# Kernel optimization log

Hardware: AMD Instinct MI355X
Metric: run time of the kernel (lower is better)

## Reference

```python
import jax, jax.numpy as jnp
import numpy as np
import math

INPUT_SIZE = 1024
B, L1, L2 = 8, 2048, 2048


def setup_inputs() -> dict:
    key = jax.random.key(0)
    ks = jax.random.split(key, 10)
    s = 1.0 / math.sqrt(INPUT_SIZE)
    return {
        "Q": jax.random.normal(ks[0], (B, L1, INPUT_SIZE), dtype=jnp.float32),
        "K": jax.random.normal(ks[1], (B, L2, INPUT_SIZE), dtype=jnp.float32),
        "V": jax.random.normal(ks[2], (B, L2, INPUT_SIZE), dtype=jnp.float32),
        "K_mask": jax.random.randint(ks[3], (B, L2), 0, 2, dtype=jnp.int32),
        "Wq": jax.random.normal(ks[4], (INPUT_SIZE, INPUT_SIZE), dtype=jnp.float32) * s,
        "bq": jax.random.normal(ks[5], (INPUT_SIZE,), dtype=jnp.float32) * s,
        "Wk": jax.random.normal(ks[6], (INPUT_SIZE, INPUT_SIZE), dtype=jnp.float32) * s,
        "bk": jax.random.normal(ks[7], (INPUT_SIZE,), dtype=jnp.float32) * s,
        "Wv": jax.random.normal(ks[8], (INPUT_SIZE, INPUT_SIZE), dtype=jnp.float32) * s,
        "bv": jax.random.normal(ks[9], (INPUT_SIZE,), dtype=jnp.float32) * s,
    }


def reference(Q, K, V, K_mask, Wq, bq, Wk, bk, Wv, bv):
    # Linear projections (torch Linear: x @ W.T + b)
    q = jnp.einsum('bld,ed->ble', Q, Wq) + bq
    k = jnp.einsum('bld,ed->ble', K, Wk) + bk
    v = jnp.einsum('bld,ed->ble', V, Wv) + bv
    # scores: [B, L1, L2], scaled by sqrt(input_size)
    scores = jnp.einsum('bqd,bkd->bqk', q, k) / math.sqrt(INPUT_SIZE)
    # K_mask == 1 marks padding -> -inf before softmax
    scores = jnp.where(K_mask[:, None, :] == 1, -jnp.inf, scores)
    alpha = jax.nn.softmax(scores, axis=-1)
    matched_seq = jnp.einsum('bqk,bkd->bqd', alpha, v)
    return matched_seq
```

## Files before the change

### kernel.cpp

```cpp
#include <hip/hip_runtime.h>


using u16 = unsigned short;
using frag_ab = __attribute__((ext_vector_type(8))) short;
using frag_cd = __attribute__((ext_vector_type(4))) float;

#define BAR() asm volatile("s_barrier" ::: "memory")
#define WAITV(n) asm volatile("s_waitcnt vmcnt(" #n ")" ::: "memory")
#define WAITLGKM0() do { asm volatile("s_waitcnt lgkmcnt(0)" ::: "memory"); \
                         __builtin_amdgcn_sched_barrier(0); } while (0)
#define HINT_LGKM8() asm volatile("s_waitcnt lgkmcnt(8)" ::: "memory")
#define L(d, ab, h) (lds + (((d) * 4) + ((ab) * 2) + (h)) * 8192)

__device__ __forceinline__ u16 f2bf(float f) {
  union { float f; unsigned u; } c; c.f = f;
  unsigned u = c.u;
  return (u16)((u + 0x7FFFu + ((u >> 16) & 1u)) >> 16);
}
__device__ __forceinline__ u16 f2h(float f) {
  union { _Float16 h; u16 u; } c; c.h = (_Float16)f; return c.u;
}
__device__ __forceinline__ float h2f(u16 u) {
  union { u16 u; _Float16 h; } c; c.u = u; return (float)c.h;
}

__device__ __forceinline__ void async_ld16(const void* g, void* l) {
  __builtin_amdgcn_global_load_lds(
      (const __attribute__((address_space(1))) unsigned*)g,
      (__attribute__((address_space(3))) unsigned*)l, 16, 0, 0);
}

__global__ void cvtw3(const float* __restrict__ a, const float* __restrict__ b,
                      const float* __restrict__ c, u16* __restrict__ out) {
  const float* in = blockIdx.z == 0 ? a : (blockIdx.z == 1 ? b : c);
  u16* o = out + (long)blockIdx.z * 1048576L;
  long i = ((long)blockIdx.x * 256 + threadIdx.x) * 4;
  float4 v = *reinterpret_cast<const float4*>(in + i);
  *reinterpret_cast<ushort4*>(o + i) =
      make_ushort4(f2bf(v.x), f2bf(v.y), f2bf(v.z), f2bf(v.w));
}

__global__ void cvt3_f32_bf16(const float* __restrict__ q, const float* __restrict__ k,
                              const float* __restrict__ v, u16* __restrict__ out) {
  const float* in = blockIdx.z == 0 ? q : (blockIdx.z == 1 ? k : v);
  u16* o = out + (long)blockIdx.z * 16777216L;
  long i = ((long)blockIdx.x * 256 + threadIdx.x) * 4;
  float4 x = *reinterpret_cast<const float4*>(in + i);
  *reinterpret_cast<ushort4*>(o + i) =
      make_ushort4(f2bf(x.x), f2bf(x.y), f2bf(x.z), f2bf(x.w));
}

__device__ __forceinline__ void stage_half(const u16* __restrict__ g_rowbase,
                                           long Kstr, u16* l_half,
                                           int wave, int lane) {
  const int t = wave * 64 + lane;
  #pragma unroll
  for (int i = 0; i < 2; i++) {
    const int row = i * 64 + (t >> 3);
    const int cb  = (t & 7) * 16;
    const int cbs = cb ^ ((row & 7) << 4);
    async_ld16(g_rowbase + (long)row * Kstr + (cbs >> 1),
               l_half + i * 4096 + wave * 512);
  }
}

__device__ __forceinline__ frag_ab ld_frag(const u16* half_base, int r, int k) {
  const int idx = r * 64 + (k ^ ((r & 7) << 3));
  return *reinterpret_cast<const frag_ab*>(half_base + idx);
}

struct SwzOut { int z, m0, n0; };
__device__ __forceinline__ SwzOut grid_swizzle() {
  const int gx = gridDim.x, gy = gridDim.y, gz = gridDim.z;
  const int nwg = gx * gy * gz;
  const int lin = ((int)blockIdx.z * gy + blockIdx.y) * gx + blockIdx.x;
  const int q8 = nwg >> 3, r8 = nwg & 7;
  const int xcd = lin & 7, idx8 = lin >> 3;
  const int swz = (xcd < r8 ? xcd * (q8 + 1) : r8 * (q8 + 1) + (xcd - r8) * q8) + idx8;
  SwzOut o;
  o.z = swz / (gx * gy);
  const int rem = swz % (gx * gy);
  o.m0 = (rem / gx) * 256;
  o.n0 = (rem % gx) * 256;
  return o;
}

__device__ __forceinline__ void
gemm256_core(int out_mode, const u16* __restrict__ Ab, const u16* __restrict__ Bb,
             void* __restrict__ Cb, const float* __restrict__ bias,
             int N, int K, int m0, int n0, float scale, u16* lds)
{
  const int tid = threadIdx.x;
  const int wave = tid >> 6, lane = tid & 63;
  const int wm = wave >> 2, wn = wave & 3;
  const int ln15 = lane & 15, kof = (lane >> 4) * 8;
  const int rB0 = (wn & 1) * 64;
  const int NT = K >> 6;

  frag_cd acc[8][4];
  #pragma unroll
  for (int i = 0; i < 8; i++)
    #pragma unroll
    for (int j = 0; j < 4; j++)
      acc[i][j] = (frag_cd){0.f, 0.f, 0.f, 0.f};

  stage_half(Ab + (long)(m0 +   0) * K, K, L(0, 0, 0), wave, lane);
  stage_half(Ab + (long)(m0 + 128) * K, K, L(0, 0, 1), wave, lane);
  stage_half(Bb + (long)(n0 +   0) * K, K, L(0, 1, 0), wave, lane);
  stage_half(Bb + (long)(n0 + 128) * K, K, L(0, 1, 1), wave, lane);
  {
    const int t1 = (1 < NT) ? 1 : 0;
    stage_half(Bb + (long)(n0 +   0) * K + t1 * 64, K, L(1, 1, 0), wave, lane);
    stage_half(Bb + (long)(n0 + 128) * K + t1 * 64, K, L(1, 1, 1), wave, lane);
  }
  WAITV(4);
  BAR();

  for (int t = 0; t < NT; ++t) {
    const int d = t & 1;
    const u16* Al = L(d, 0, wm);
    const u16* Bl = L(d, 1, wn >> 1);
    const int tA = (t + 1 < NT) ? t + 1 : NT - 1;
    const int tB = (t + 2 < NT) ? t + 2 : NT - 1;

    frag_ab bf[4][2], af[2][2];

    #pragma unroll
    for (int bn = 0; bn < 4; ++bn)
      #pragma unroll
      for (int kk = 0; kk < 2; ++kk)
        bf[bn][kk] = ld_frag(Bl, rB0 + bn * 16 + ln15, kk * 32 + kof);
    #pragma unroll
    for (int am = 0; am < 2; ++am)
      #pragma unroll
      for (int kk = 0; kk < 2; ++kk)
        af[am][kk] = ld_frag(Al, am * 16 + ln15, kk * 32 + kof);
    stage_half(Ab + (long)(m0 + 0) * K + tA * 64, K, L(d ^ 1, 0, 0), wave, lane);
    HINT_LGKM8();
    BAR();
    __builtin_amdgcn_s_setprio(1);
    #pragma unroll
    for (int am = 0; am < 2; ++am)
      #pragma unroll
      for (int bn = 0; bn < 4; ++bn)
        #pragma unroll
        for (int kk = 0; kk < 2; ++kk)
          acc[am][bn] = __builtin_amdgcn_mfma_f32_16x16x32_bf16(af[am][kk], bf[bn][kk], acc[am][bn], 0, 0, 0);
    __builtin_amdgcn_s_setprio(0);
    BAR();

    #pragma unroll
    for (int am = 0; am < 2; ++am)
      #pragma unroll
      for (int kk = 0; kk < 2; ++kk)
        af[am][kk] = ld_frag(Al, (2 + am) * 16 + ln15, kk * 32 + kof);
    stage_half(Ab + (long)(m0 + 128) * K + tA * 64, K, L(d ^ 1, 0, 1), wave, lane);
    BAR();
    __builtin_amdgcn_s_setprio(1);
    #pragma unroll
    for (int am = 0; am < 2; ++am)
      #pragma unroll
      for (int bn = 0; bn < 4; ++bn)
        #pragma unroll
        for (int kk = 0; kk < 2; ++kk)
          acc[2 + am][bn] = __builtin_amdgcn_mfma_f32_16x16x32_bf16(af[am][kk], bf[bn][kk], acc[2 + am][bn], 0, 0, 0);
    __builtin_amdgcn_s_setprio(0);
    BAR();

    #pragma unroll
    for (int am = 0; am < 2; ++am)
      #pragma unroll
      for (int kk = 0; kk < 2; ++kk)
        af[am][kk] = ld_frag(Al, (4 + am) * 16 + ln15, kk * 32 + kof);
    stage_half(Bb + (long)(n0 + 0) * K + tB * 64, K, L(d, 1, 0), wave, lane);
    BAR();
    __builtin_amdgcn_s_setprio(1);
    #pragma unroll
    for (int am = 0; am < 2; ++am)
      #pragma unroll
      for (int bn = 0; bn < 4; ++bn)
        #pragma unroll
        for (int kk = 0; kk < 2; ++kk)
          acc[4 + am][bn] = __builtin_amdgcn_mfma_f32_16x16x32_bf16(af[am][kk], bf[bn][kk], acc[4 + am][bn], 0, 0, 0);
    __builtin_amdgcn_s_setprio(0);
    BAR();

    #pragma unroll
    for (int am = 0; am < 2; ++am)
      #pragma unroll
      for (int kk = 0; kk < 2; ++kk)
        af[am][kk] = ld_frag(Al, (6 + am) * 16 + ln15, kk * 32 + kof);
    stage_half(Bb + (long)(n0 + 128) * K + tB * 64, K, L(d, 1, 1), wave, lane);
    BAR();
    __builtin_amdgcn_s_setprio(1);
    #pragma unroll
    for (int am = 0; am < 2; ++am)
      #pragma unroll
      for (int bn = 0; bn < 4; ++bn)
        #pragma unroll
        for (int kk = 0; kk < 2; ++kk)
          acc[6 + am][bn] = __builtin_amdgcn_mfma_f32_16x16x32_bf16(af[am][kk], bf[bn][kk], acc[6 + am][bn], 0, 0, 0);
    __builtin_amdgcn_s_setprio(0);
    WAITV(4);
    BAR();
  }

  WAITV(0);
  BAR();

  const int cl = lane & 15;
  const int rb = (lane >> 4) * 4;

  if (out_mode == 1 || out_mode == 3) {
    u16* Wt = lds + wave * 8192;
    #pragma unroll
    for (int am = 0; am < 8; ++am)
      #pragma unroll
      for (int bn = 0; bn < 4; ++bn) {
        const int col = bn * 16 + cl;
        const float badd = bias ? bias[n0 + wn * 64 + col] : 0.f;
        #pragma unroll
        for (int r = 0; r < 4; ++r) {
          const int row = am * 16 + rb + r;
          const int slot = (col >> 3) ^ ((row >> 2) & 7);
          const float val = acc[am][bn][r] * scale + badd;
          Wt[row * 64 + slot * 8 + (col & 7)] = (out_mode == 1) ? f2bf(val) : f2h(val);
        }
      }
    WAITLGKM0();
    u16* Cp = (u16*)Cb;
    #pragma unroll
    for (int i = 0; i < 16; ++i) {
      const int row = (lane >> 3) + i * 8;
      const int c = lane & 7;
      const int slot = c ^ ((row >> 2) & 7);
      frag_ab v = *reinterpret_cast<const frag_ab*>(Wt + row * 64 + slot * 8);
      const long grow = m0 + wm * 128 + row;
      const int gcol = n0 + wn * 64 + c * 8;
      *reinterpret_cast<frag_ab*>(Cp + grow * N + gcol) = v;
    }
  } else if (out_mode == 0) {
    float* Wt = (float*)(void*)lds + wave * 4096;
    float* Cp = (float*)Cb;
    #pragma unroll
    for (int p = 0; p < 2; ++p) {
      #pragma unroll
      for (int am = 0; am < 8; ++am)
        #pragma unroll
        for (int bn = 0; bn < 2; ++bn) {
          const int col = bn * 16 + cl;
          #pragma unroll
          for (int r = 0; r < 4; ++r) {
            const int row = am * 16 + rb + r;
            const int slot = (col >> 2) ^ ((row >> 2) & 7);
            Wt[row * 32 + slot * 4 + (col & 3)] = acc[am][2 * p + bn][r] * scale;
          }
        }
      WAITLGKM0();
      #pragma unroll
      for (int i = 0; i < 16; ++i) {
        const int row = (lane >> 3) + i * 8;
        const int c = lane & 7;
        const int slot = c ^ ((row >> 2) & 7);
        float4 v = *reinterpret_cast<const float4*>(Wt + row * 32 + slot * 4);
        const long grow = m0 + wm * 128 + row;
        const int gcol = n0 + wn * 64 + p * 32 + c * 4;
        *reinterpret_cast<float4*>(Cp + grow * N + gcol) = v;
      }
      if (p == 0) WAITLGKM0();
    }
  } else {
    #pragma unroll
    for (int bn = 0; bn < 4; ++bn) {
      const int gcol = n0 + wn * 64 + bn * 16 + cl;
      const float badd = bias ? bias[gcol] : 0.f;
      #pragma unroll
      for (int am = 0; am < 8; ++am) {
        const int grow0 = m0 + wm * 128 + am * 16 + rb;
        ushort4 pk;
        pk.x = f2bf(acc[am][bn][0] * scale + badd);
        pk.y = f2bf(acc[am][bn][1] * scale + badd);
        pk.z = f2bf(acc[am][bn][2] * scale + badd);
        pk.w = f2bf(acc[am][bn][3] * scale + badd);
        const int bb = grow0 >> 11, l2 = grow0 & 2047;
        *reinterpret_cast<ushort4*>((u16*)Cb + ((long)bb * N + gcol) * 2048L + l2) = pk;
      }
    }
  }
}

__global__ void __launch_bounds__(512, 2)
proj3_gemm(const u16* __restrict__ X, const u16* __restrict__ Wb,
           const float* __restrict__ bq, const float* __restrict__ bk,
           const float* __restrict__ bv, u16* __restrict__ qkb,
           u16* __restrict__ vT)
{
  __shared__ u16 lds[8 * 8192];
  SwzOut s = grid_swizzle();
  const u16* A = X + (long)s.z * 16777216L;
  const u16* W = Wb + (long)s.z * 1048576L;
  const float* bias = s.z == 0 ? bq : (s.z == 1 ? bk : bv);
  if (s.z < 2)
    gemm256_core(1, A, W, qkb + (long)s.z * 16777216L, bias,
                 1024, 1024, s.m0, s.n0, 1.f, lds);
  else
    gemm256_core(2, A, W, vT, bias, 1024, 1024, s.m0, s.n0, 1.f, lds);
}

__global__ void __launch_bounds__(512, 2)
proj1_gemm(int mode, const u16* A, const u16* W, void* C, const float* bias) {
  __shared__ u16 lds[8 * 8192];
  SwzOut s = grid_swizzle();
  gemm256_core(mode, A, W, C, bias, 1024, 1024, s.m0, s.n0, 1.f, lds);
}

__global__ void __launch_bounds__(512, 2)
qk_gemm(const u16* A, const u16* Bt, void* C,
        int M, int N, int K, long sA, long sB, long sC, float scale) {
  __shared__ u16 lds[8 * 8192];
  SwzOut s = grid_swizzle();
  gemm256_core(3, A + (long)s.z * sA, Bt + (long)s.z * sB,
               (u16*)C + (long)s.z * sC, nullptr, N, K, s.m0, s.n0, scale, lds);
}
__global__ void __launch_bounds__(512, 2)
pv_gemm(const u16* A, const u16* Bt, void* C,
        int M, int N, int K, long sA, long sB, long sC, float scale) {
  __shared__ u16 lds[8 * 8192];
  SwzOut s = grid_swizzle();
  gemm256_core(0, A + (long)s.z * sA, Bt + (long)s.z * sB,
               (float*)C + (long)s.z * sC, nullptr, N, K, s.m0, s.n0, scale, lds);
}

__global__ void softmax_rows_h(const u16* __restrict__ S, const int* __restrict__ Km,
                               u16* __restrict__ P)
{
  const long row = blockIdx.x;
  const int b = (int)(row >> 11);
  const u16* s = S + row * 2048;
  const int* mask = Km + (long)b * 2048;
  u16* p = P + row * 2048;

  const int t = threadIdx.x;
  const int base = t * 8;

  ushort4 r0 = *reinterpret_cast<const ushort4*>(s + base);
  ushort4 r1 = *reinterpret_cast<const ushort4*>(s + base + 4);
  int4 mA = *reinterpret_cast<const int4*>(mask + base);
  int4 mB = *reinterpret_cast<const int4*>(mask + base + 4);

  float vals[8] = {h2f(r0.x), h2f(r0.y), h2f(r0.z), h2f(r0.w),
                   h2f(r1.x), h2f(r1.y), h2f(r1.z), h2f(r1.w)};
  const int mk[8] = {mA.x, mA.y, mA.z, mA.w, mB.x, mB.y, mB.z, mB.w};

  float mx = -3.0e38f;
  #pragma unroll
  for (int i = 0; i < 8; i++) if (!mk[i]) mx = fmaxf(mx, vals[i]);
  #pragma unroll
  for (int off = 32; off > 0; off >>= 1) mx = fmaxf(mx, __shfl_xor(mx, off));

  __shared__ float redm[4], reds[4];
  const int wave = t >> 6, lane = t & 63;
  if (lane == 0) redm[wave] = mx;
  __syncthreads();
  mx = fmaxf(fmaxf(redm[0], redm[1]), fmaxf(redm[2], redm[3]));

  float e[8]; float sum = 0.f;
  #pragma unroll
  for (int i = 0; i < 8; i++) { e[i] = mk[i] ? 0.f : __expf(vals[i] - mx); sum += e[i]; }
  #pragma unroll
  for (int off = 32; off > 0; off >>= 1) sum += __shfl_xor(sum, off);
  if (lane == 0) reds[wave] = sum;
  __syncthreads();
  sum = reds[0] + reds[1] + reds[2] + reds[3];
  const float inv = 1.f / sum;

  *reinterpret_cast<ushort4*>(p + base) =
      make_ushort4(f2bf(e[0]*inv), f2bf(e[1]*inv), f2bf(e[2]*inv), f2bf(e[3]*inv));
  *reinterpret_cast<ushort4*>(p + base + 4) =
      make_ushort4(f2bf(e[4]*inv), f2bf(e[5]*inv), f2bf(e[6]*inv), f2bf(e[7]*inv));
}

extern "C" void kernel_launch(void* const* d_in, const int* in_sizes, int n_in,
                              void* d_out, int out_size, void* d_ws, size_t ws_size,
                              hipStream_t stream) {
  (void)in_sizes; (void)n_in; (void)out_size;

  const float* Qin  = (const float*)d_in[0];
  const float* Kin  = (const float*)d_in[1];
  const float* Vin  = (const float*)d_in[2];
  const int*   Kmask = (const int*)d_in[3];
  const float* Wq = (const float*)d_in[4];
  const float* bq = (const float*)d_in[5];
  const float* Wk = (const float*)d_in[6];
  const float* bk = (const float*)d_in[7];
  const float* Wv = (const float*)d_in[8];
  const float* bv = (const float*)d_in[9];

  char* ws = (char*)d_ws;
  const size_t MB = 1024UL * 1024UL;
  const dim3 blk(256);
  const dim3 gblk(512);
  const float rs = 0.03125f;

  if (ws_size >= 226 * MB) {
    u16*  qb = (u16*)(ws);
    u16*  vT = (u16*)(ws + 64 * MB);
    u16*  P  = (u16*)(ws + 96 * MB);
    u16*  Xq = (u16*)(ws + 96 * MB);
    u16*  S  = (u16*)(ws + 160 * MB);
    u16*  Wb = (u16*)(ws + 224 * MB);

    cvt3_f32_bf16<<<dim3(16384, 1, 3), blk, 0, stream>>>(Qin, Kin, Vin, Xq);
    cvtw3<<<dim3(1024, 1, 3), blk, 0, stream>>>(Wq, Wk, Wv, Wb);

    proj3_gemm<<<dim3(4, 64, 3), gblk, 0, stream>>>(Xq, Wb, bq, bk, bv, qb, vT);

    qk_gemm<<<dim3(8, 8, 8), gblk, 0, stream>>>(qb, qb + 16777216L, S,
        2048, 2048, 1024, 2048L * 1024, 2048L * 1024, 2048L * 2048, rs);
    softmax_rows_h<<<dim3(16384), blk, 0, stream>>>(S, Kmask, P);

    pv_gemm<<<dim3(4, 8, 8), gblk, 0, stream>>>(P, vT, d_out,
        2048, 1024, 2048, 2048L * 2048, 1024L * 2048, 2048L * 1024, 1.f);
  } else if (ws_size >= 194 * MB) {
    u16*  qb = (u16*)(ws);
    u16*  vT = (u16*)(ws + 64 * MB);
    u16*  P  = (u16*)(ws + 96 * MB);
    u16*  Xq = (u16*)(ws + 96 * MB);
    u16*  S  = (u16*)(ws + 160 * MB);
    u16*  Wb = (u16*)(ws + 186 * MB);

    cvt3_f32_bf16<<<dim3(16384, 1, 3), blk, 0, stream>>>(Qin, Kin, Vin, Xq);
    cvtw3<<<dim3(1024, 1, 3), blk, 0, stream>>>(Wq, Wk, Wv, Wb);

    proj3_gemm<<<dim3(4, 64, 3), gblk, 0, stream>>>(Xq, Wb, bq, bk, bv, qb, vT);

    for (int h = 0; h < 2; h++) {
      const u16* qbH = qb + (long)(4 * h) * 2048 * 1024;
      const u16* kbH = qb + 16777216L + (long)(4 * h) * 2048 * 1024;
      qk_gemm<<<dim3(8, 8, 4), gblk, 0, stream>>>(qbH, kbH, S,
          2048, 2048, 1024, 2048L * 1024, 2048L * 1024, 2048L * 2048, rs);
      softmax_rows_h<<<dim3(8192), blk, 0, stream>>>(
          S, Kmask + (long)(4 * h) * 2048, P + (long)(4 * h) * 2048 * 2048);
    }

    pv_gemm<<<dim3(4, 8, 8), gblk, 0, stream>>>(P, vT, d_out,
        2048, 1024, 2048, 2048L * 2048, 1024L * 2048, 2048L * 1024, 1.f);
  } else {
    u16*  qb = (u16*)(ws);
    u16*  kb = (u16*)(ws + 32 * MB);
    u16*  vT = (u16*)(ws + 64 * MB);
    u16*  Xb = (u16*)(ws + 96 * MB);
    u16*  S  = (u16*)(ws + 96 * MB);
    u16*  P  = (u16*)(ws + 104 * MB);
    u16*  Wb = (u16*)(ws + 128 * MB);

    cvtw3<<<dim3(1024, 1, 3), blk, 0, stream>>>(Wq, Wk, Wv, Wb);
    cvt3_f32_bf16<<<dim3(16384, 1, 1), blk, 0, stream>>>(Qin, Qin, Qin, Xb);
    proj1_gemm<<<dim3(4, 64, 1), gblk, 0, stream>>>(1, Xb, Wb, qb, bq);
    cvt3_f32_bf16<<<dim3(16384, 1, 1), blk, 0, stream>>>(Kin, Kin, Kin, Xb);
    proj1_gemm<<<dim3(4, 64, 1), gblk, 0, stream>>>(1, Xb, Wb + 1048576L, kb, bk);
    cvt3_f32_bf16<<<dim3(16384, 1, 1), blk, 0, stream>>>(Vin, Vin, Vin, Xb);
    proj1_gemm<<<dim3(4, 64, 1), gblk, 0, stream>>>(2, Xb, Wb + 2L * 1048576L, vT, bv);

    for (int b = 0; b < 8; b++) {
      const u16* qbB = qb + (long)b * 2048 * 1024;
      const u16* kbB = kb + (long)b * 2048 * 1024;
      const u16* vTB = vT + (long)b * 1024 * 2048;
      float* outB = (float*)d_out + (long)b * 2048 * 1024;

      qk_gemm<<<dim3(8, 8, 1), gblk, 0, stream>>>(qbB, kbB, S,
          2048, 2048, 1024, 0, 0, 0, rs);
      softmax_rows_h<<<dim3(2048), blk, 0, stream>>>(S, Kmask + (long)b * 2048, P);
      pv_gemm<<<dim3(4, 8, 1), gblk, 0, stream>>>(P, vTB, outB,
          2048, 1024, 2048, 0, 0, 0, 1.f);
    }
  }
}
```

Measured before the change: 329.9 us.

## Fuse fp32-to-bf16 input conversion into the projection GEMM

Removes the separate pass that converted Q, K and V from fp32 to bf16. The new projection kernel stages fp32 tiles into LDS and converts them to bf16 in registers while building MFMA fragments. This avoids writing and rereading 96MB of bf16 intermediates, at the cost of twice the LDS traffic for the A operand, triple-buffered LDS and one block per CU. The shared GEMM core also reorders its global staging, issuing both A halves together, and the fallback workspace layouts shrink.

```diff
diff --git a/kernel.cpp b/kernel.cpp
--- a/kernel.cpp
+++ b/kernel.cpp
@@ -1,4 +1,5 @@
 #include <hip/hip_runtime.h>
+#include <hip/hip_bf16.h>
 
 
 using u16 = unsigned short;
@@ -9,7 +10,6 @@
 #define WAITV(n) asm volatile("s_waitcnt vmcnt(" #n ")" ::: "memory")
 #define WAITLGKM0() do { asm volatile("s_waitcnt lgkmcnt(0)" ::: "memory"); \
                          __builtin_amdgcn_sched_barrier(0); } while (0)
-#define HINT_LGKM8() asm volatile("s_waitcnt lgkmcnt(8)" ::: "memory")
 #define L(d, ab, h) (lds + (((d) * 4) + ((ab) * 2) + (h)) * 8192)
 
 __device__ __forceinline__ u16 f2bf(float f) {
@@ -22,6 +22,17 @@
 }
 __device__ __forceinline__ float h2f(u16 u) {
   union { u16 u; _Float16 h; } c; c.u = u; return (float)c.h;
+}
+
+__device__ __forceinline__ frag_ab pack8f(float4 a, float4 b) {
+  union { __hip_bfloat162 h; unsigned u; } c0, c1, c2, c3;
+  c0.h = __float22bfloat162_rn(make_float2(a.x, a.y));
+  c1.h = __float22bfloat162_rn(make_float2(a.z, a.w));
+  c2.h = __float22bfloat162_rn(make_float2(b.x, b.y));
+  c3.h = __float22bfloat162_rn(make_float2(b.z, b.w));
+  union { frag_ab f; unsigned u[4]; } r;
+  r.u[0] = c0.u; r.u[1] = c1.u; r.u[2] = c2.u; r.u[3] = c3.u;
+  return r.f;
 }
 
 __device__ __forceinline__ void async_ld16(const void* g, void* l) {
@@ -40,16 +51,6 @@
       make_ushort4(f2bf(v.x), f2bf(v.y), f2bf(v.z), f2bf(v.w));
 }
 
-__global__ void cvt3_f32_bf16(const float* __restrict__ q, const float* __restrict__ k,
-                              const float* __restrict__ v, u16* __restrict__ out) {
-  const float* in = blockIdx.z == 0 ? q : (blockIdx.z == 1 ? k : v);
-  u16* o = out + (long)blockIdx.z * 16777216L;
-  long i = ((long)blockIdx.x * 256 + threadIdx.x) * 4;
-  float4 x = *reinterpret_cast<const float4*>(in + i);
-  *reinterpret_cast<ushort4*>(o + i) =
-      make_ushort4(f2bf(x.x), f2bf(x.y), f2bf(x.z), f2bf(x.w));
-}
-
 __device__ __forceinline__ void stage_half(const u16* __restrict__ g_rowbase,
                                            long Kstr, u16* l_half,
                                            int wave, int lane) {
@@ -64,9 +65,25 @@
   }
 }
 
+__device__ __forceinline__ void stage_f32(const float* __restrict__ g, int hsel,
+                                          float* dst, int tid) {
+  #pragma unroll
+  for (int i = 0; i < 4; i++) {
+    const int rp = i * 32 + (tid >> 4);
+    const int row = (rp & 63) + ((rp >> 6) << 7) + hsel * 64;
+    const int ss = (tid & 15) ^ (rp & 7);
+    async_ld16(g + (long)row * 1024 + ss * 4,
+               dst + i * 2048 + (tid >> 6) * 256);
+  }
+}
+
 __device__ __forceinline__ frag_ab ld_frag(const u16* half_base, int r, int k) {
   const int idx = r * 64 + (k ^ ((r & 7) << 3));
   return *reinterpret_cast<const frag_ab*>(half_base + idx);
+}
+
+__device__ __forceinline__ float4 ld4f(const float* half, int rp, int s) {
+  return *reinterpret_cast<const float4*>(half + rp * 64 + ((s ^ (rp & 7)) << 2));
 }
 
 struct SwzOut { int z, m0, n0; };
@@ -85,6 +102,18 @@
   return o;
 }
 
+#define MFMA_PAIR(base)                                                        \
+  __builtin_amdgcn_s_setprio(1);                                              \
+  _Pragma("unroll")                                                           \
+  for (int am = 0; am < 2; ++am)                                              \
+    _Pragma("unroll")                                                         \
+    for (int bn = 0; bn < 4; ++bn)                                            \
+      _Pragma("unroll")                                                       \
+      for (int kk = 0; kk < 2; ++kk)                                          \
+        acc[(base) + am][bn] = __builtin_amdgcn_mfma_f32_16x16x32_bf16(       \
+            af[am][kk], bf[bn][kk], acc[(base) + am][bn], 0, 0, 0);           \
+  __builtin_amdgcn_s_setprio(0);
+
 __device__ __forceinline__ void
 gemm256_core(int out_mode, const u16* __restrict__ Ab, const u16* __restrict__ Bb,
              void* __restrict__ Cb, const float* __restrict__ bias,
@@ -135,18 +164,10 @@
       #pragma unroll
       for (int kk = 0; kk < 2; ++kk)
         af[am][kk] = ld_frag(Al, am * 16 + ln15, kk * 32 + kof);
-    stage_half(Ab + (long)(m0 + 0) * K + tA * 64, K, L(d ^ 1, 0, 0), wave, lane);
-    HINT_LGKM8();
-    BAR();
-    __builtin_amdgcn_s_setprio(1);
-    #pragma unroll
-    for (int am = 0; am < 2; ++am)
-      #pragma unroll
-      for (int bn = 0; bn < 4; ++bn)
-        #pragma unroll
-        for (int kk = 0; kk < 2; ++kk)
-          acc[am][bn] = __builtin_amdgcn_mfma_f32_16x16x32_bf16(af[am][kk], bf[bn][kk], acc[am][bn], 0, 0, 0);
-    __builtin_amdgcn_s_setprio(0);
+    stage_half(Ab + (long)(m0 +   0) * K + tA * 64, K, L(d ^ 1, 0, 0), wave, lane);
+    stage_half(Ab + (long)(m0 + 128) * K + tA * 64, K, L(d ^ 1, 0, 1), wave, lane);
+    BAR();
+    MFMA_PAIR(0)
     BAR();
 
     #pragma unroll
@@ -154,17 +175,9 @@
       #pragma unroll
       for (int kk = 0; kk < 2; ++kk)
         af[am][kk] = ld_frag(Al, (2 + am) * 16 + ln15, kk * 32 + kof);
-    stage_half(Ab + (long)(m0 + 128) * K + tA * 64, K, L(d ^ 1, 0, 1), wave, lane);
-    BAR();
-    __builtin_amdgcn_s_setprio(1);
-    #pragma unroll
-    for (int am = 0; am < 2; ++am)
-      #pragma unroll
-      for (int bn = 0; bn < 4; ++bn)
-        #pragma unroll
-        for (int kk = 0; kk < 2; ++kk)
-          acc[2 + am][bn] = __builtin_amdgcn_mfma_f32_16x16x32_bf16(af[am][kk], bf[bn][kk], acc[2 + am][bn], 0, 0, 0);
-    __builtin_amdgcn_s_setprio(0);
+    stage_half(Bb + (long)(n0 + 0) * K + tB * 64, K, L(d, 1, 0), wave, lane);
+    BAR();
+    MFMA_PAIR(2)
     BAR();
 
     #pragma unroll
@@ -172,17 +185,9 @@
       #pragma unroll
       for (int kk = 0; kk < 2; ++kk)
         af[am][kk] = ld_frag(Al, (4 + am) * 16 + ln15, kk * 32 + kof);
-    stage_half(Bb + (long)(n0 + 0) * K + tB * 64, K, L(d, 1, 0), wave, lane);
-    BAR();
-    __builtin_amdgcn_s_setprio(1);
-    #pragma unroll
-    for (int am = 0; am < 2; ++am)
-      #pragma unroll
-      for (int bn = 0; bn < 4; ++bn)
-        #pragma unroll
-        for (int kk = 0; kk < 2; ++kk)
-          acc[4 + am][bn] = __builtin_amdgcn_mfma_f32_16x16x32_bf16(af[am][kk], bf[bn][kk], acc[4 + am][bn], 0, 0, 0);
-    __builtin_amdgcn_s_setprio(0);
+    stage_half(Bb + (long)(n0 + 128) * K + tB * 64, K, L(d, 1, 1), wave, lane);
+    BAR();
+    MFMA_PAIR(4)
     BAR();
 
     #pragma unroll
@@ -190,17 +195,8 @@
       #pragma unroll
       for (int kk = 0; kk < 2; ++kk)
         af[am][kk] = ld_frag(Al, (6 + am) * 16 + ln15, kk * 32 + kof);
-    stage_half(Bb + (long)(n0 + 128) * K + tB * 64, K, L(d, 1, 1), wave, lane);
-    BAR();
-    __builtin_amdgcn_s_setprio(1);
-    #pragma unroll
-    for (int am = 0; am < 2; ++am)
-      #pragma unroll
-      for (int bn = 0; bn < 4; ++bn)
-        #pragma unroll
-        for (int kk = 0; kk < 2; ++kk)
-          acc[6 + am][bn] = __builtin_amdgcn_mfma_f32_16x16x32_bf16(af[am][kk], bf[bn][kk], acc[6 + am][bn], 0, 0, 0);
-    __builtin_amdgcn_s_setprio(0);
+    BAR();
+    MFMA_PAIR(6)
     WAITV(4);
     BAR();
   }
@@ -211,20 +207,18 @@
   const int cl = lane & 15;
   const int rb = (lane >> 4) * 4;
 
-  if (out_mode == 1 || out_mode == 3) {
+  if (out_mode == 3) {
     u16* Wt = lds + wave * 8192;
     #pragma unroll
     for (int am = 0; am < 8; ++am)
       #pragma unroll
       for (int bn = 0; bn < 4; ++bn) {
         const int col = bn * 16 + cl;
-        const float badd = bias ? bias[n0 + wn * 64 + col] : 0.f;
         #pragma unroll
         for (int r = 0; r < 4; ++r) {
           const int row = am * 16 + rb + r;
           const int slot = (col >> 3) ^ ((row >> 2) & 7);
-          const float val = acc[am][bn][r] * scale + badd;
-          Wt[row * 64 + slot * 8 + (col & 7)] = (out_mode == 1) ? f2bf(val) : f2h(val);
+          Wt[row * 64 + slot * 8 + (col & 7)] = f2h(acc[am][bn][r] * scale);
         }
       }
     WAITLGKM0();
@@ -239,7 +233,7 @@
       const int gcol = n0 + wn * 64 + c * 8;
       *reinterpret_cast<frag_ab*>(Cp + grow * N + gcol) = v;
     }
-  } else if (out_mode == 0) {
+  } else {
     float* Wt = (float*)(void*)lds + wave * 4096;
     float* Cp = (float*)Cb;
     #pragma unroll
@@ -269,49 +263,7 @@
       }
       if (p == 0) WAITLGKM0();
     }
-  } else {
-    #pragma unroll
-    for (int bn = 0; bn < 4; ++bn) {
-      const int gcol = n0 + wn * 64 + bn * 16 + cl;
-      const float badd = bias ? bias[gcol] : 0.f;
-      #pragma unroll
-      for (int am = 0; am < 8; ++am) {
-        const int grow0 = m0 + wm * 128 + am * 16 + rb;
-        ushort4 pk;
-        pk.x = f2bf(acc[am][bn][0] * scale + badd);
-        pk.y = f2bf(acc[am][bn][1] * scale + badd);
-        pk.z = f2bf(acc[am][bn][2] * scale + badd);
-        pk.w = f2bf(acc[am][bn][3] * scale + badd);
-        const int bb = grow0 >> 11, l2 = grow0 & 2047;
-        *reinterpret_cast<ushort4*>((u16*)Cb + ((long)bb * N + gcol) * 2048L + l2) = pk;
-      }
-    }
-  }
-}
-
-__global__ void __launch_bounds__(512, 2)
-proj3_gemm(const u16* __restrict__ X, const u16* __restrict__ Wb,
-           const float* __restrict__ bq, const float* __restrict__ bk,
-           const float* __restrict__ bv, u16* __restrict__ qkb,
-           u16* __restrict__ vT)
-{
-  __shared__ u16 lds[8 * 8192];
-  SwzOut s = grid_swizzle();
-  const u16* A = X + (long)s.z * 16777216L;
-  const u16* W = Wb + (long)s.z * 1048576L;
-  const float* bias = s.z == 0 ? bq : (s.z == 1 ? bk : bv);
-  if (s.z < 2)
-    gemm256_core(1, A, W, qkb + (long)s.z * 16777216L, bias,
-                 1024, 1024, s.m0, s.n0, 1.f, lds);
-  else
-    gemm256_core(2, A, W, vT, bias, 1024, 1024, s.m0, s.n0, 1.f, lds);
-}
-
-__global__ void __launch_bounds__(512, 2)
-proj1_gemm(int mode, const u16* A, const u16* W, void* C, const float* bias) {
-  __shared__ u16 lds[8 * 8192];
-  SwzOut s = grid_swizzle();
-  gemm256_core(mode, A, W, C, bias, 1024, 1024, s.m0, s.n0, 1.f, lds);
+  }
 }
 
 __global__ void __launch_bounds__(512, 2)
@@ -329,6 +281,169 @@
   SwzOut s = grid_swizzle();
   gemm256_core(0, A + (long)s.z * sA, Bt + (long)s.z * sB,
                (float*)C + (long)s.z * sC, nullptr, N, K, s.m0, s.n0, scale, lds);
+}
+
+#define AFP(s) ((float*)(void*)lds + (s) * 8192)
+#define BHP(s) (lds + 49152 + (s) * 8192)
+
+__global__ void __launch_bounds__(512, 1)
+proj3f_gemm(const float* __restrict__ Qf, const float* __restrict__ Kf,
+            const float* __restrict__ Vf, const u16* __restrict__ Wb,
+            const float* __restrict__ bq, const float* __restrict__ bk,
+            const float* __restrict__ bv, u16* __restrict__ qkb,
+            u16* __restrict__ vT)
+{
+  __shared__ u16 lds[73728];
+
+  SwzOut s = grid_swizzle();
+  const float* Af = s.z == 0 ? Qf : (s.z == 1 ? Kf : Vf);
+  const u16* W = Wb + (long)s.z * 1048576L;
+  const float* bias = s.z == 0 ? bq : (s.z == 1 ? bk : bv);
+  const int m0 = s.m0, n0 = s.n0;
+  const float* Atile = Af + (long)m0 * 1024;
+
+  const int tid = threadIdx.x;
+  const int wave = tid >> 6, lane = tid & 63;
+  const int wm = wave >> 2, wn = wave & 3;
+  const int ln15 = lane & 15, kof = (lane >> 4) * 8;
+  const int rB0 = (wn & 1) * 64;
+
+  frag_cd acc[8][4];
+  #pragma unroll
+  for (int i = 0; i < 8; i++)
+    #pragma unroll
+    for (int j = 0; j < 4; j++)
+      acc[i][j] = (frag_cd){0.f, 0.f, 0.f, 0.f};
+
+  stage_f32(Atile, 0, AFP(0), tid);
+  stage_half(W + (long)(n0 +   0) * 1024, 1024, BHP(0), wave, lane);
+  stage_half(W + (long)(n0 + 128) * 1024, 1024, BHP(1), wave, lane);
+  stage_f32(Atile, 1, AFP(1), tid);
+  WAITV(4);
+  BAR();
+
+  int a0 = 0, a1 = 1, a2 = 2;
+  for (int t = 0; t < 16; ++t) {
+    const int tn = (t + 1 < 16) ? t + 1 : 15;
+    const float* Al0 = AFP(a0);
+    const float* Al1 = AFP(a1);
+    const u16* Bl = BHP((wn >> 1) ? a1 : a0);
+
+    frag_ab bf[4][2], af[2][2];
+
+    #pragma unroll
+    for (int bn = 0; bn < 4; ++bn)
+      #pragma unroll
+      for (int kk = 0; kk < 2; ++kk)
+        bf[bn][kk] = ld_frag(Bl, rB0 + bn * 16 + ln15, kk * 32 + kof);
+    #pragma unroll
+    for (int am = 0; am < 2; ++am)
+      #pragma unroll
+      for (int kk = 0; kk < 2; ++kk) {
+        const int rp = wm * 64 + am * 16 + ln15;
+        const int s0 = (kk * 32 + kof) >> 2;
+        af[am][kk] = pack8f(ld4f(Al0, rp, s0), ld4f(Al0, rp, s0 + 1));
+      }
+    stage_f32(Atile + tn * 64, 0, AFP(a2), tid);
+    BAR();
+    MFMA_PAIR(0)
+    BAR();
+
+    #pragma unroll
+    for (int am = 0; am < 2; ++am)
+      #pragma unroll
+      for (int kk = 0; kk < 2; ++kk) {
+        const int rp = wm * 64 + (2 + am) * 16 + ln15;
+        const int s0 = (kk * 32 + kof) >> 2;
+        af[am][kk] = pack8f(ld4f(Al0, rp, s0), ld4f(Al0, rp, s0 + 1));
+      }
+    stage_half(W + (long)(n0 + 0) * 1024 + tn * 64, 1024, BHP(a2), wave, lane);
+    BAR();
+    MFMA_PAIR(2)
+    WAITV(6);
+    BAR();
+
+    #pragma unroll
+    for (int am = 0; am < 2; ++am)
+      #pragma unroll
+      for (int kk = 0; kk < 2; ++kk) {
+        const int rp = wm * 64 + am * 16 + ln15;
+        const int s0 = (kk * 32 + kof) >> 2;
+        af[am][kk] = pack8f(ld4f(Al1, rp, s0), ld4f(Al1, rp, s0 + 1));
+      }
+    stage_half(W + (long)(n0 + 128) * 1024 + tn * 64, 1024, BHP(a0), wave, lane);
+    stage_f32(Atile + tn * 64, 1, AFP(a0), tid);
+    BAR();
+    MFMA_PAIR(4)
+    BAR();
+
+    #pragma unroll
+    for (int am = 0; am < 2; ++am)
+      #pragma unroll
+      for (int kk = 0; kk < 2; ++kk) {
+        const int rp = wm * 64 + (2 + am) * 16 + ln15;
+        const int s0 = (kk * 32 + kof) >> 2;
+        af[am][kk] = pack8f(ld4f(Al1, rp, s0), ld4f(Al1, rp, s0 + 1));
+      }
+    BAR();
+    MFMA_PAIR(6)
+    WAITV(4);
+    BAR();
+
+    const int tmp = a0; a0 = a2; a2 = a1; a1 = tmp;
+  }
+
+  WAITV(0);
+  BAR();
+
+  const int cl = lane & 15;
+  const int rb = (lane >> 4) * 4;
+
+  if (s.z < 2) {
+    u16* Wt = lds + wave * 8192;
+    #pragma unroll
+    for (int am = 0; am < 8; ++am)
+      #pragma unroll
+      for (int bn = 0; bn < 4; ++bn) {
+        const int col = bn * 16 + cl;
+        const float badd = bias[n0 + wn * 64 + col];
+        #pragma unroll
+        for (int r = 0; r < 4; ++r) {
+          const int row = am * 16 + rb + r;
+          const int slot = (col >> 3) ^ ((row >> 2) & 7);
+          Wt[row * 64 + slot * 8 + (col & 7)] = f2bf(acc[am][bn][r] + badd);
+        }
+      }
+    WAITLGKM0();
+    u16* Cp = qkb + (long)s.z * 16777216L;
+    #pragma unroll
+    for (int i = 0; i < 16; ++i) {
+      const int row = (lane >> 3) + i * 8;
+      const int c = lane & 7;
+      const int slot = c ^ ((row >> 2) & 7);
+      frag_ab v = *reinterpret_cast<const frag_ab*>(Wt + row * 64 + slot * 8);
+      const long grow = m0 + wm * 128 + row;
+      const int gcol = n0 + wn * 64 + c * 8;
+      *reinterpret_cast<frag_ab*>(Cp + grow * 1024 + gcol) = v;
+    }
+  } else {
+    #pragma unroll
+    for (int bn = 0; bn < 4; ++bn) {
+      const int gcol = n0 + wn * 64 + bn * 16 + cl;
+      const float badd = bias[gcol];
+      #pragma unroll
+      for (int am = 0; am < 8; ++am) {
+        const int grow0 = m0 + wm * 128 + am * 16 + rb;
+        ushort4 pk;
+        pk.x = f2bf(acc[am][bn][0] + badd);
+        pk.y = f2bf(acc[am][bn][1] + badd);
+        pk.z = f2bf(acc[am][bn][2] + badd);
+        pk.w = f2bf(acc[am][bn][3] + badd);
+        const int bb = grow0 >> 11, l2 = grow0 & 2047;
+        *reinterpret_cast<ushort4*>(vT + ((long)bb * 1024 + gcol) * 2048L + l2) = pk;
+      }
+    }
+  }
 }
 
 __global__ void softmax_rows_h(const u16* __restrict__ S, const int* __restrict__ Km,
@@ -406,14 +521,12 @@
     u16*  qb = (u16*)(ws);
     u16*  vT = (u16*)(ws + 64 * MB);
     u16*  P  = (u16*)(ws + 96 * MB);
-    u16*  Xq = (u16*)(ws + 96 * MB);
     u16*  S  = (u16*)(ws + 160 * MB);
     u16*  Wb = (u16*)(ws + 224 * MB);
 
-    cvt3_f32_bf16<<<dim3(16384, 1, 3), blk, 0, stream>>>(Qin, Kin, Vin, Xq);
     cvtw3<<<dim3(1024, 1, 3), blk, 0, stream>>>(Wq, Wk, Wv, Wb);
-
-    proj3_gemm<<<dim3(4, 64, 3), gblk, 0, stream>>>(Xq, Wb, bq, bk, bv, qb, vT);
+    proj3f_gemm<<<dim3(4, 64, 3), gblk, 0, stream>>>(Qin, Kin, Vin, Wb,
+        bq, bk, bv, qb, vT);
 
     qk_gemm<<<dim3(8, 8, 8), gblk, 0, stream>>>(qb, qb + 16777216L, S,
         2048, 2048, 1024, 2048L * 1024, 2048L * 1024, 2048L * 2048, rs);
@@ -421,50 +534,42 @@
 
     pv_gemm<<<dim3(4, 8, 8), gblk, 0, stream>>>(P, vT, d_out,
         2048, 1024, 2048, 2048L * 2048, 1024L * 2048, 2048L * 1024, 1.f);
-  } else if (ws_size >= 194 * MB) {
+  } else if (ws_size >= 182 * MB) {
     u16*  qb = (u16*)(ws);
     u16*  vT = (u16*)(ws + 64 * MB);
     u16*  P  = (u16*)(ws + 96 * MB);
-    u16*  Xq = (u16*)(ws + 96 * MB);
     u16*  S  = (u16*)(ws + 160 * MB);
-    u16*  Wb = (u16*)(ws + 186 * MB);
-
-    cvt3_f32_bf16<<<dim3(16384, 1, 3), blk, 0, stream>>>(Qin, Kin, Vin, Xq);
+    u16*  Wb = (u16*)(ws + 176 * MB);
+
     cvtw3<<<dim3(1024, 1, 3), blk, 0, stream>>>(Wq, Wk, Wv, Wb);
-
-    proj3_gemm<<<dim3(4, 64, 3), gblk, 0, stream>>>(Xq, Wb, bq, bk, bv, qb, vT);
-
-    for (int h = 0; h < 2; h++) {
-      const u16* qbH = qb + (long)(4 * h) * 2048 * 1024;
-      const u16* kbH = qb + 16777216L + (long)(4 * h) * 2048 * 1024;
-      qk_gemm<<<dim3(8, 8, 4), gblk, 0, stream>>>(qbH, kbH, S,
+    proj3f_gemm<<<dim3(4, 64, 3), gblk, 0, stream>>>(Qin, Kin, Vin, Wb,
+        bq, bk, bv, qb, vT);
+
+    for (int h = 0; h < 4; h++) {
+      const u16* qbH = qb + (long)(2 * h) * 2048 * 1024;
+      const u16* kbH = qb + 16777216L + (long)(2 * h) * 2048 * 1024;
+      qk_gemm<<<dim3(8, 8, 2), gblk, 0, stream>>>(qbH, kbH, S,
           2048, 2048, 1024, 2048L * 1024, 2048L * 1024, 2048L * 2048, rs);
-      softmax_rows_h<<<dim3(8192), blk, 0, stream>>>(
-          S, Kmask + (long)(4 * h) * 2048, P + (long)(4 * h) * 2048 * 2048);
+      softmax_rows_h<<<dim3(4096), blk, 0, stream>>>(
+          S, Kmask + (long)(2 * h) * 2048, P + (long)(2 * h) * 2048 * 2048);
     }
 
     pv_gemm<<<dim3(4, 8, 8), gblk, 0, stream>>>(P, vT, d_out,
         2048, 1024, 2048, 2048L * 2048, 1024L * 2048, 2048L * 1024, 1.f);
   } else {
     u16*  qb = (u16*)(ws);
-    u16*  kb = (u16*)(ws + 32 * MB);
     u16*  vT = (u16*)(ws + 64 * MB);
-    u16*  Xb = (u16*)(ws + 96 * MB);
     u16*  S  = (u16*)(ws + 96 * MB);
     u16*  P  = (u16*)(ws + 104 * MB);
-    u16*  Wb = (u16*)(ws + 128 * MB);
+    u16*  Wb = (u16*)(ws + 112 * MB);
 
     cvtw3<<<dim3(1024, 1, 3), blk, 0, stream>>>(Wq, Wk, Wv, Wb);
-    cvt3_f32_bf16<<<dim3(16384, 1, 1), blk, 0, stream>>>(Qin, Qin, Qin, Xb);
-    proj1_gemm<<<dim3(4, 64, 1), gblk, 0, stream>>>(1, Xb, Wb, qb, bq);
-    cvt3_f32_bf16<<<dim3(16384, 1, 1), blk, 0, stream>>>(Kin, Kin, Kin, Xb);
-    proj1_gemm<<<dim3(4, 64, 1), gblk, 0, stream>>>(1, Xb, Wb + 1048576L, kb, bk);
-    cvt3_f32_bf16<<<dim3(16384, 1, 1), blk, 0, stream>>>(Vin, Vin, Vin, Xb);
-    proj1_gemm<<<dim3(4, 64, 1), gblk, 0, stream>>>(2, Xb, Wb + 2L * 1048576L, vT, bv);
+    proj3f_gemm<<<dim3(4, 64, 3), gblk, 0, stream>>>(Qin, Kin, Vin, Wb,
+        bq, bk, bv, qb, vT);
 
     for (int b = 0; b < 8; b++) {
       const u16* qbB = qb + (long)b * 2048 * 1024;
-      const u16* kbB = kb + (long)b * 2048 * 1024;
+      const u16* kbB = qb + 16777216L + (long)b * 2048 * 1024;
       const u16* vTB = vT + (long)b * 1024 * 2048;
       float* outB = (float*)d_out + (long)b * 2048 * 1024;
 
```

Result: slower. 372.6 us (+12.9%).
